# Optimization experiments

Hardware: AMD Instinct MI355X
Metric: run time of the kernel (lower is better)

## Reference

```python
import jax, jax.numpy as jnp
import numpy as np

T, B, C = 256, 32, 64          # max_time, batch, num_classes
BEAM, TOP = 16, 4              # beam_width, top_paths
BLANK = 0                      # blank_index
NEG = -1e9                     # soft -inf (keeps grads NaN-free)


def setup_inputs() -> dict:
    key = jax.random.key(0)
    k1, k2 = jax.random.split(key)
    data = jax.random.normal(k1, (T, B, C), dtype=jnp.float32)
    data_length = jax.random.randint(k2, (B,), 1, T + 1, dtype=jnp.int32)
    return {"data": data, "data_length": data_length}


def _decode_one(logp, length):
    """Graves-style CTC prefix beam search for one sample.
    logp: [T, C] log-probs, length: scalar number of valid frames.
    Beam state: padded label seqs, lengths, log p(ending in blank),
    log p(ending in non-blank), two rolling prefix hashes (for duplicate-prefix
    merging), and an 'active' flag."""
    classes = jnp.arange(C)
    seqs0 = jnp.full((BEAM, T), -1, jnp.int32)
    lens0 = jnp.zeros((BEAM,), jnp.int32)
    p_b0 = jnp.full((BEAM,), NEG, jnp.float32).at[0].set(0.0)  # empty prefix
    p_nb0 = jnp.full((BEAM,), NEG, jnp.float32)
    h1_0 = jnp.zeros((BEAM,), jnp.uint32)
    h2_0 = jnp.zeros((BEAM,), jnp.uint32)
    act0 = jnp.zeros((BEAM,), bool).at[0].set(True)

    def step(state, inp):
        seqs, lens, p_b, p_nb, h1, h2, act = state
        lp, t = inp                                   # lp: [C]
        tot = jnp.logaddexp(p_b, p_nb)                # [BEAM]
        last = seqs[jnp.arange(BEAM), jnp.maximum(lens - 1, 0)]
        last = jnp.where(lens > 0, last, -1)
        # ---- 'stay' candidates: same prefix (blank, or repeat of last char) ----
        stay_pb = tot + lp[BLANK]
        stay_pnb = jnp.where(lens > 0, p_nb + lp[jnp.maximum(last, 0)], NEG)
        # ---- 'extend' candidates: prefix + c, c != blank ----
        # repeat char only extends via a blank-ending path (p_b)
        base = jnp.where(classes[None, :] == last[:, None], p_b[:, None], tot[:, None])
        ext = base + lp[None, :]                      # [BEAM, C]
        ext = jnp.where((classes[None, :] == BLANK) | (~act[:, None]), NEG, ext)
        cc = (classes[None, :] + 1).astype(jnp.uint32)
        ch1 = h1[:, None] * jnp.uint32(1000003) + cc  # [BEAM, C]
        ch2 = h2[:, None] * jnp.uint32(69069) + cc
        # merge: extend(i,c) equal to an existing active beam j folds into j's p_nb
        match = ((ch1[:, :, None] == h1[None, None, :])
                 & (ch2[:, :, None] == h2[None, None, :])
                 & act[None, None, :])                # [BEAM, C, BEAM]
        merged = jax.nn.logsumexp(jnp.where(match, ext[:, :, None], NEG), axis=(0, 1))
        stay_pnb = jnp.logaddexp(stay_pnb, merged)
        ext = jnp.where(match.any(-1), NEG, ext)
        # ---- prune: top BEAM among BEAM stays + BEAM*C extends ----
        stay_tot = jnp.logaddexp(stay_pb, stay_pnb)
        scores = jnp.concatenate([stay_tot, ext.reshape(-1)])
        vals, idx = jax.lax.top_k(scores, BEAM)
        is_stay = idx < BEAM
        parent = jnp.where(is_stay, idx, (idx - BEAM) // C)
        c_new = jnp.where(is_stay, 0, (idx - BEAM) % C)
        plen = lens[parent]
        n_seqs = seqs[parent]
        put = (jnp.arange(T)[None, :] == plen[:, None]) & (~is_stay)[:, None]
        n_seqs = jnp.where(put, c_new[:, None].astype(jnp.int32), n_seqs)
        n_lens = plen + (~is_stay).astype(jnp.int32)
        n_pb = jnp.where(is_stay, stay_pb[parent], NEG)
        n_pnb = jnp.where(is_stay, stay_pnb[parent], vals)
        n_h1 = jnp.where(is_stay, h1[parent], ch1[parent, c_new])
        n_h2 = jnp.where(is_stay, h2[parent], ch2[parent, c_new])
        n_act = vals > NEG / 2
        live = t < length                             # freeze state past data_length
        new_state = tuple(jnp.where(live, n, o) for n, o in zip(
            (n_seqs, n_lens, n_pb, n_pnb, n_h1, n_h2, n_act),
            (seqs, lens, p_b, p_nb, h1, h2, act)))
        return new_state, None

    state, _ = jax.lax.scan(step, (seqs0, lens0, p_b0, p_nb0, h1_0, h2_0, act0),
                            (logp, jnp.arange(T)))
    seqs, lens, p_b, p_nb, _, _, _ = state
    tot = jnp.logaddexp(p_b, p_nb)
    top_tot, order = jax.lax.top_k(tot, TOP)
    # (neg log prob, label length, decoded labels padded with -1)
    return -top_tot, lens[order], seqs[order]


def reference(data, data_length):
    logp = jax.nn.log_softmax(data, axis=-1)          # from_logits=True
    logp = jnp.transpose(logp, (1, 0, 2))             # [B, T, C]
    probs, lengths, labels = jax.vmap(_decode_one)(logp, data_length)
    return probs, lengths, labels
```

## Files before the change

kernel.cpp:

```cpp
#include <hip/hip_runtime.h>


#define T_MAX 256
#define BATCH 32
#define NC 64
#define BEAM 16
#define TOPK 4
#define NEG (-1.0e9f)
#define BIGNEG (-2.0e9f)
#define FLTMAX 3.402823466e+38f

typedef unsigned long long u64;
typedef unsigned int u32;

__device__ __forceinline__ float log_add_exp(float a, float b) {
    float m = fmaxf(a, b);
    float d = fabsf(a - b);
    return m + log1pf(expf(-d));
}

__device__ __forceinline__ u32 rdl_u32(u32 v, int sl) {
    return (u32)__builtin_amdgcn_readlane((int)v, sl);
}
__device__ __forceinline__ float rdl_f(float v, int sl) {
    return __uint_as_float(rdl_u32(__float_as_uint(v), sl));
}
__device__ __forceinline__ int rdl_i(int v, int sl) {
    return __builtin_amdgcn_readlane(v, sl);
}
__device__ __forceinline__ u32 mbcnt64(u64 m) {
    return __builtin_amdgcn_mbcnt_hi((u32)(m >> 32),
           __builtin_amdgcn_mbcnt_lo((u32)m, 0u));
}

__device__ __forceinline__ u64 pack_key_fl(float v, u32 fl) {
    u32 u = __float_as_uint(v);
    u32 m = u ^ ((u32)((int)u >> 31) | 0x80000000u);
    return ((u64)m << 11) | (u64)fl;
}
__device__ __forceinline__ u64 pack_key(float v, int flat) {
    return pack_key_fl(v, (u32)(2047 - flat));
}
__device__ __forceinline__ float key_val(u64 key) {
    u32 k = (u32)(key >> 11);
    u32 u = (k & 0x80000000u) ? (k ^ 0x80000000u) : ~k;
    return __uint_as_float(u);
}
__device__ __forceinline__ int key_flat(u64 key) {
    return 2047 - (int)(key & 2047u);
}
__device__ __forceinline__ u64 max64(u64 a, u64 b) { return a > b ? a : b; }
__device__ __forceinline__ u64 min64(u64 a, u64 b) { return a < b ? a : b; }

__device__ __forceinline__ void sort16_desc_u64(u64 (&a)[BEAM]) {
    #pragma unroll
    for (int k = 2; k <= 16; k <<= 1) {
        #pragma unroll
        for (int j = k >> 1; j > 0; j >>= 1) {
            #pragma unroll
            for (int i = 0; i < 16; ++i) {
                int l = i ^ j;
                if (l > i) {
                    const bool desc = ((i & k) == 0);
                    u64 x = a[i], y = a[l];
                    bool sw = desc ? (x < y) : (x > y);
                    a[i] = sw ? y : x;
                    a[l] = sw ? x : y;
                }
            }
        }
    }
}

__device__ __forceinline__ void sort16_desc_f32(float (&a)[BEAM]) {
    #pragma unroll
    for (int k = 2; k <= 16; k <<= 1) {
        #pragma unroll
        for (int j = k >> 1; j > 0; j >>= 1) {
            #pragma unroll
            for (int i = 0; i < 16; ++i) {
                int l = i ^ j;
                if (l > i) {
                    const bool desc = ((i & k) == 0);
                    float x = a[i], y = a[l];
                    float mx = fmaxf(x, y), mn = fminf(x, y);
                    a[i] = desc ? mx : mn;
                    a[l] = desc ? mn : mx;
                }
            }
        }
    }
}

template <int M>
__device__ __forceinline__ void bf_level_f32(float (&a)[BEAM]) {
    float c[BEAM];
    #pragma unroll
    for (int i = 0; i < BEAM; ++i)
        c[i] = __shfl_xor(a[BEAM - 1 - i], M, 64);
    #pragma unroll
    for (int i = 0; i < BEAM; ++i)
        c[i] = fmaxf(a[i], c[i]);
    #pragma unroll
    for (int j = 8; j > 0; j >>= 1) {
        #pragma unroll
        for (int i = 0; i < BEAM; ++i)
            if ((i & j) == 0) {
                float x = c[i], y = c[i | j];
                c[i]     = fmaxf(x, y);
                c[i | j] = fminf(x, y);
            }
    }
    #pragma unroll
    for (int i = 0; i < BEAM; ++i) a[i] = c[i];
}

__global__ __launch_bounds__(64) void softmax_kernel(const float* __restrict__ data,
                                                     float* __restrict__ lp_out,
                                                     float* __restrict__ rm_out) {
    const int row = blockIdx.x;
    const int lane = threadIdx.x;
    float x = data[row * NC + lane];
    float mx = x;
    #pragma unroll
    for (int m = 1; m < 64; m <<= 1) mx = fmaxf(mx, __shfl_xor(mx, m, 64));
    float sum = expf(x - mx);
    #pragma unroll
    for (int m = 1; m < 64; m <<= 1) sum += __shfl_xor(sum, m, 64);
    float ls = logf(sum);
    lp_out[row * NC + lane] = (x - mx) - ls;
    if (lane == 0) rm_out[row] = -ls;
}

template <bool PRE>
__global__ __launch_bounds__(64, 1) void ctc_beam_kernel(
        const float* __restrict__ data,
        const float* __restrict__ lp_pre,
        const float* __restrict__ rm_pre,
        const int*   __restrict__ data_len,
        float*       __restrict__ out)
{
    const int b    = blockIdx.x;
    const int lane = threadIdx.x;

    __shared__ __align__(16) u64 slotsL[128];
    __shared__ unsigned short hist[T_MAX * BEAM];
    __shared__ int ord4[TOPK];
    __shared__ float val4[TOPK];

    int len = data_len[b];
    if (len < 0) len = 0;
    if (len > T_MAX) len = T_MAX;

    float pb  = (lane == 0) ? 0.0f : NEG;
    float pnb = NEG;
    float tot = log_add_exp(pb, pnb);
    u32 h1 = 0u, h2 = 0u;
    u32 ph1 = 0u, ph2 = 0u;
    int lenb = 0, lastb = -1;
    float spread = 1.0e30f;
    float v1prev = 0.0f;

    const float* src = PRE ? lp_pre : data;
    float xpref = (len > 0) ? src[b * NC + lane] : 0.f;
    float rmpref = (PRE && len > 0) ? rm_pre[b] : 0.f;

    #pragma unroll 1
    for (int t = 0; t < len; ++t) {
        float x = xpref;
        float rm = rmpref;
        int tn = (t + 1 < len) ? (t + 1) : t;
        xpref = src[(tn * BATCH + b) * NC + lane];
        if (PRE) rmpref = rm_pre[tn * BATCH + b];

        slotsL[lane] = 0ull;

        float lp;
        if (PRE) {
            lp = x;
        } else {
            float mx = x;
            #pragma unroll
            for (int m = 1; m < 64; m <<= 1) mx = fmaxf(mx, __shfl_xor(mx, m, 64));
            float sum = expf(x - mx);
            #pragma unroll
            for (int m = 1; m < 64; m <<= 1) sum += __shfl_xor(sum, m, 64);
            float ls = logf(sum);
            lp = (x - mx) - ls;
            rm = -ls;
        }
        float lp0 = rdl_f(lp, 0);

        int lastc = (lastb < 0) ? 0 : (lastb & 63);
        float lplast = __shfl(lp, lastc, 64);
        float st_pb   = tot + lp0;
        float st_pnb0 = (lenb > 0) ? (pnb + lplast) : NEG;

        u32 p2 = (h2 & 0x03FFFFFFu) | ((u32)(lastb & 63) << 26);
        u32 ph2m = ph2 & 0x03FFFFFFu;
        float lpx = (lane == 0) ? BIGNEG : lp;

        float e0s[BEAM];
        int mi = -1;
        #pragma unroll
        for (int i = 0; i < BEAM; ++i) {
            float tot_i = rdl_f(tot, i);
            float pb_i  = rdl_f(pb, i);
            u32   h1_i  = rdl_u32(h1, i);
            u32   p2_i  = rdl_u32(p2, i);
            int last_i = (int)(p2_i >> 26);
            float e0  = tot_i + lpx;
            float e0f = pb_i + lpx;
            e0s[i] = (lane == last_i) ? e0f : e0;
            if (ph1 == h1_i && ph2m == (p2_i & 0x03FFFFFFu)) mi = i;
        }

        bool jm = (lane < BEAM) && (lenb > 0) && (mi >= 0);
        u64 mm = __ballot(jm);
        float merged = NEG;
        float st_pnb;
        if (mm) {
            u32 excl = 0u;
            int mpack = ((mi & 15) << 6) | (lastb & 63);
            u64 mw = mm;
            while (mw) {
                int j = (int)__builtin_ctzll(mw);
                mw &= mw - 1;
                int pk = rdl_i(mpack, j);
                int i  = (pk >> 6) & 15;
                int c  = pk & 63;
                float tot_i = rdl_f(tot, i);
                float pb_i  = rdl_f(pb, i);
                int   l_i   = rdl_i(lastb, i);
                float lp_c  = rdl_f(lp, c);
                float mv = ((c == l_i) ? pb_i : tot_i) + lp_c;
                if (lane == j) merged = mv;
                if (lane == c) excl |= (1u << i);
            }
            #pragma unroll
            for (int s = 0; s < BEAM; ++s)
                if ((excl >> s) & 1u) e0s[s] = BIGNEG;
            st_pnb = log_add_exp(st_pnb0, merged);
        } else {
            st_pnb = st_pnb0;
        }
        float st_tot = log_add_exp(st_pb, st_pnb);

        auto do_scatter = [&](float th) -> u32 {
            u32 mycnt = 0;
            #pragma unroll
            for (int s = 0; s < BEAM; ++s) mycnt += (e0s[s] >= th) ? 1u : 0u;
            bool stw = (lane < BEAM) && (st_tot >= th);
            mycnt += stw ? 1u : 0u;
            u32 base = 0;
            #pragma unroll
            for (int k = 0; k < 5; ++k)
                base += mbcnt64(__ballot(((mycnt >> k) & 1u) != 0u)) << k;
            u32 totc = rdl_u32(base + mycnt, 63);
            u32 pos = base;
            u32 dump = (64u + (u32)lane) << 3;
            u32 fl = 2031u - (u32)lane;
            #pragma unroll
            for (int s = 0; s < BEAM; ++s) {
                bool w = (e0s[s] >= th) && (pos < 64u);
                u32 a = w ? (pos << 3) : dump;
                *(u64*)((char*)slotsL + a) = pack_key_fl(e0s[s], fl);
                pos += (e0s[s] >= th) ? 1u : 0u;
                fl -= 64u;
            }
            {
                u32 a = (stw && pos < 64u) ? (pos << 3) : dump;
                *(u64*)((char*)slotsL + a) = pack_key_fl(st_tot, 2047u - (u32)lane);
            }
            return totc;
        };

        float A = v1prev + rm;
        u32 totc = do_scatter(A - spread);
        if (totc < BEAM || totc > 32u) {
            float th2 = (totc > 32u) ? (A - 0.45f * spread)
                                     : (A - (2.5f * spread + 1.0f));
            slotsL[lane] = 0ull;
            asm volatile("" ::: "memory");
            totc = do_scatter(th2);
            if (totc < BEAM || totc > 32u) {
                float a[BEAM];
                #pragma unroll
                for (int s = 0; s < BEAM; ++s) a[s] = e0s[s];
                sort16_desc_f32(a);
                {
                    float sv = (lane < BEAM) ? st_tot : NEG;
                    #pragma unroll
                    for (int i = BEAM - 1; i >= 1; --i)
                        a[i] = fmaxf(a[i], fminf(a[i - 1], sv));
                    a[0] = fmaxf(a[0], sv);
                }
                bf_level_f32<1>(a);  bf_level_f32<2>(a);  bf_level_f32<4>(a);
                bf_level_f32<8>(a);  bf_level_f32<16>(a); bf_level_f32<32>(a);
                slotsL[lane] = 0ull;
                asm volatile("" ::: "memory");
                totc = do_scatter(a[15]);
            }
        }

        int flat; float val;
        if (totc <= 32u) {
            asm volatile("" ::: "memory");
            u64 mk = slotsL[lane];
            u32 rank = 0;
            const uint4* q4 = (const uint4*)slotsL;
            if (totc <= 16u) {
                #pragma unroll
                for (int q = 0; q < 8; ++q) {
                    uint4 w = q4[q];
                    u64 ka = ((u64)w.y << 32) | w.x;
                    u64 kb = ((u64)w.w << 32) | w.z;
                    rank += (ka > mk) ? 1u : 0u;
                    rank += (kb > mk) ? 1u : 0u;
                }
            } else {
                #pragma unroll
                for (int q = 0; q < 16; ++q) {
                    uint4 w = q4[q];
                    u64 ka = ((u64)w.y << 32) | w.x;
                    u64 kb = ((u64)w.w << 32) | w.z;
                    rank += (ka > mk) ? 1u : 0u;
                    rank += (kb > mk) ? 1u : 0u;
                }
            }
            int selhi = 0, sello = 0;
            if (lane < (int)totc) {
                selhi = __builtin_amdgcn_ds_permute((int)(rank << 2),
                                                    (int)(mk >> 32));
                sello = __builtin_amdgcn_ds_permute((int)(rank << 2),
                                                    (int)(mk & 0xFFFFFFFFu));
            }
            u64 sel = ((u64)(u32)selhi << 32) | (u32)sello;
            flat = key_flat(sel);
            val  = key_val(sel);
        } else {
            u64 ku[BEAM];
            #pragma unroll
            for (int s = 0; s < BEAM; ++s)
                ku[s] = pack_key(e0s[s], BEAM + s * NC + lane);
            sort16_desc_u64(ku);
            u64 sk = (lane < BEAM) ? pack_key(st_tot, lane) : 0ull;
            #pragma unroll
            for (int i = BEAM - 1; i >= 1; --i)
                ku[i] = max64(ku[i], min64(ku[i - 1], sk));
            ku[0] = max64(ku[0], sk);
            #pragma unroll 1
            for (int m = 1; m < 64; m <<= 1) {
                u64 c_[BEAM];
                #pragma unroll
                for (int i = 0; i < BEAM; ++i) {
                    u64 o = (u64)__shfl_xor((long long)ku[BEAM - 1 - i], m, 64);
                    c_[i] = max64(ku[i], o);
                }
                #pragma unroll
                for (int j = 8; j > 0; j >>= 1) {
                    #pragma unroll
                    for (int i = 0; i < BEAM; ++i)
                        if ((i & j) == 0) {
                            u64 xk = c_[i], yk = c_[i | j];
                            bool sw = xk < yk;
                            c_[i]     = sw ? yk : xk;
                            c_[i | j] = sw ? xk : yk;
                        }
                }
                #pragma unroll
                for (int i = 0; i < BEAM; ++i) ku[i] = c_[i];
            }
            u64 selkey = ku[0];
            #pragma unroll
            for (int i = 1; i < BEAM; ++i)
                if (lane == i) selkey = ku[i];
            flat = key_flat(selkey);
            val  = key_val(selkey);
        }

        {
            float v1n  = rdl_f(val, 0);
            float v16n = rdl_f(val, 15);
            spread = (fmaxf(A, v1n) - v16n) * 1.25f + 1.0e-3f;
            v1prev = v1n;
        }

        bool stay = flat < BEAM;
        int pidx = (stay ? flat : ((flat - BEAM) >> 6)) & 15;
        int cnew = stay ? 0 : ((flat - BEAM) & 63);

        float g_stpb  = __shfl(st_pb, pidx, 64);
        float g_stpnb = __shfl(st_pnb, pidx, 64);
        u32   g_h1    = (u32)__shfl((int)h1, pidx, 64);
        u32   g_h2    = (u32)__shfl((int)h2, pidx, 64);
        u32   g_ph1   = (u32)__shfl((int)ph1, pidx, 64);
        u32   g_ph2   = (u32)__shfl((int)ph2, pidx, 64);
        int   g_ll    = __shfl((lenb << 8) | (lastb & 255), pidx, 64);
        int   g_len   = g_ll >> 8;
        int   g_last  = (int)(signed char)(g_ll & 255);

        pb   = stay ? g_stpb : NEG;
        pnb  = stay ? g_stpnb : val;
        tot  = val;
        ph1  = stay ? g_ph1 : g_h1;
        ph2  = stay ? g_ph2 : g_h2;
        h1   = stay ? g_h1 : (g_h1 * 1000003u + (u32)(cnew + 1));
        h2   = stay ? g_h2 : (g_h2 * 69069u   + (u32)(cnew + 1));
        lenb = g_len + (stay ? 0 : 1);
        lastb = stay ? g_last : cnew;
        if (lane < BEAM)
            hist[t * BEAM + lane] =
                (unsigned short)((pidx << 8) | (stay ? 0x80 : 0) | cnew);
    }
    __syncthreads();

    float ft = (lane < BEAM) ? log_add_exp(pb, pnb) : -FLTMAX;
    int fidx = (lane < BEAM) ? lane : 0x7FFFFFFF;
    for (int k = 0; k < TOPK; ++k) {
        float bv = ft; int bi = fidx;
        #pragma unroll
        for (int m = 1; m < 64; m <<= 1) {
            float ov = __shfl_xor(bv, m, 64);
            int   oi = __shfl_xor(bi, m, 64);
            if (ov > bv || (ov == bv && oi < bi)) { bv = ov; bi = oi; }
        }
        if (lane == 0) { ord4[k] = bi; val4[k] = bv; }
        if (lane == bi) ft = -FLTMAX;
    }
    __syncthreads();

    int bsel = ord4[lane & 3] & 15;
    int lensel = __shfl(lenb, bsel, 64);

    for (int e2 = lane; e2 < TOPK * T_MAX; e2 += 64)
        out[BATCH * TOPK * 2 + b * (TOPK * T_MAX) + e2] = -1.0f;
    __syncthreads();
    if (lane < TOPK) {
        const int k = lane;
        out[b * TOPK + k] = -val4[k];
        out[BATCH * TOPK + b * TOPK + k] = (float)lensel;
        int pos = lensel - 1;
        int cur = ord4[k];
        float* lab = out + BATCH * TOPK * 2 + b * (TOPK * T_MAX) + k * T_MAX;
        for (int tt = len - 1; tt >= 0; --tt) {
            unsigned short h = hist[tt * BEAM + cur];
            if (!(h & 0x80)) { lab[pos] = (float)(h & 0x7F); --pos; }
            cur = h >> 8;
        }
    }
}

extern "C" void kernel_launch(void* const* d_in, const int* in_sizes, int n_in,
                              void* d_out, int out_size, void* d_ws, size_t ws_size,
                              hipStream_t stream) {
    const float* data = (const float*)d_in[0];
    const int* data_len = (const int*)d_in[1];
    float* out = (float*)d_out;
    const size_t lp_bytes = (size_t)T_MAX * BATCH * NC * sizeof(float);
    const size_t rm_bytes = (size_t)T_MAX * BATCH * sizeof(float);
    if (ws_size >= lp_bytes + rm_bytes) {
        float* lp_ws = (float*)d_ws;
        float* rm_ws = lp_ws + (size_t)T_MAX * BATCH * NC;
        softmax_kernel<<<dim3(T_MAX * BATCH), dim3(64), 0, stream>>>(data, lp_ws, rm_ws);
        ctc_beam_kernel<true><<<dim3(BATCH), dim3(64), 0, stream>>>(data, lp_ws, rm_ws, data_len, out);
    } else {
        ctc_beam_kernel<false><<<dim3(BATCH), dim3(64), 0, stream>>>(data, nullptr, nullptr, data_len, out);
    }
}
```

Measured before the change: 590.5 us.

## Pack beam state into fewer registers, bitmask scatter, batch softmax rows, coalesce output

Beam state now lives in a packed p2 word (26-bit hash plus last char) and a prefix mask. This drops the separate h2, ph2, lenb and lastb registers and cuts shuffles in the per-step gather. The per-lane candidate count and scatter positions come from a bitmask with popcount instead of a serial running counter. The softmax kernel processes 4 rows per 256-thread block, and label backtracking goes to shared scratch before one coalesced write of the output. Beam length is now recovered from the backtrack count, and 'has last char' is tested as lastc != 0, which relies on blank never being a last character.

```diff
diff --git a/kernel.cpp b/kernel.cpp
--- a/kernel.cpp
+++ b/kernel.cpp
@@ -9,6 +9,7 @@
 #define NEG (-1.0e9f)
 #define BIGNEG (-2.0e9f)
 #define FLTMAX 3.402823466e+38f
+#define M26 0x03FFFFFFu
 
 typedef unsigned long long u64;
 typedef unsigned int u32;
@@ -115,11 +116,11 @@
     for (int i = 0; i < BEAM; ++i) a[i] = c[i];
 }
 
-__global__ __launch_bounds__(64) void softmax_kernel(const float* __restrict__ data,
-                                                     float* __restrict__ lp_out,
-                                                     float* __restrict__ rm_out) {
-    const int row = blockIdx.x;
-    const int lane = threadIdx.x;
+__global__ __launch_bounds__(256) void softmax_kernel(const float* __restrict__ data,
+                                                      float* __restrict__ lp_out,
+                                                      float* __restrict__ rm_out) {
+    const int row = blockIdx.x * 4 + (threadIdx.x >> 6);
+    const int lane = threadIdx.x & 63;
     float x = data[row * NC + lane];
     float mx = x;
     #pragma unroll
@@ -145,8 +146,10 @@
 
     __shared__ __align__(16) u64 slotsL[128];
     __shared__ unsigned short hist[T_MAX * BEAM];
+    __shared__ unsigned char scr[TOPK * T_MAX];
     __shared__ int ord4[TOPK];
     __shared__ float val4[TOPK];
+    __shared__ int cnt4[TOPK];
 
     int len = data_len[b];
     if (len < 0) len = 0;
@@ -155,9 +158,8 @@
     float pb  = (lane == 0) ? 0.0f : NEG;
     float pnb = NEG;
     float tot = log_add_exp(pb, pnb);
-    u32 h1 = 0u, h2 = 0u;
-    u32 ph1 = 0u, ph2 = 0u;
-    int lenb = 0, lastb = -1;
+    u32 h1 = 0u, p2 = 0u;
+    u32 ph1 = 0u, ph2m = 0u;
     float spread = 1.0e30f;
     float v1prev = 0.0f;
 
@@ -191,17 +193,15 @@
         }
         float lp0 = rdl_f(lp, 0);
 
-        int lastc = (lastb < 0) ? 0 : (lastb & 63);
+        int lastc = (int)(p2 >> 26);
         float lplast = __shfl(lp, lastc, 64);
         float st_pb   = tot + lp0;
-        float st_pnb0 = (lenb > 0) ? (pnb + lplast) : NEG;
-
-        u32 p2 = (h2 & 0x03FFFFFFu) | ((u32)(lastb & 63) << 26);
-        u32 ph2m = ph2 & 0x03FFFFFFu;
+        float st_pnb0 = (lastc != 0) ? (pnb + lplast) : NEG;
+
         float lpx = (lane == 0) ? BIGNEG : lp;
 
         float e0s[BEAM];
-        int mi = -1;
+        u32 mbits = 0u;
         #pragma unroll
         for (int i = 0; i < BEAM; ++i) {
             float tot_i = rdl_f(tot, i);
@@ -209,19 +209,18 @@
             u32   h1_i  = rdl_u32(h1, i);
             u32   p2_i  = rdl_u32(p2, i);
             int last_i = (int)(p2_i >> 26);
-            float e0  = tot_i + lpx;
-            float e0f = pb_i + lpx;
-            e0s[i] = (lane == last_i) ? e0f : e0;
-            if (ph1 == h1_i && ph2m == (p2_i & 0x03FFFFFFu)) mi = i;
-        }
-
-        bool jm = (lane < BEAM) && (lenb > 0) && (mi >= 0);
+            e0s[i] = ((lane == last_i) ? pb_i : tot_i) + lpx;
+            mbits |= (ph1 == h1_i && ph2m == (p2_i & M26)) ? (1u << i) : 0u;
+        }
+
+        bool jm = (lane < BEAM) && (lastc != 0) && (mbits != 0u);
         u64 mm = __ballot(jm);
         float merged = NEG;
         float st_pnb;
         if (mm) {
             u32 excl = 0u;
-            int mpack = ((mi & 15) << 6) | (lastb & 63);
+            int mi = (int)__builtin_ctz(mbits | 0x10000u);
+            int mpack = ((mi & 15) << 6) | lastc;
             u64 mw = mm;
             while (mw) {
                 int j = (int)__builtin_ctzll(mw);
@@ -231,7 +230,7 @@
                 int c  = pk & 63;
                 float tot_i = rdl_f(tot, i);
                 float pb_i  = rdl_f(pb, i);
-                int   l_i   = rdl_i(lastb, i);
+                int   l_i   = (int)(rdl_u32(p2, i) >> 26);
                 float lp_c  = rdl_f(lp, c);
                 float mv = ((c == l_i) ? pb_i : tot_i) + lp_c;
                 if (lane == j) merged = mv;
@@ -247,29 +246,30 @@
         float st_tot = log_add_exp(st_pb, st_pnb);
 
         auto do_scatter = [&](float th) -> u32 {
-            u32 mycnt = 0;
-            #pragma unroll
-            for (int s = 0; s < BEAM; ++s) mycnt += (e0s[s] >= th) ? 1u : 0u;
+            u32 sm = 0u;
+            #pragma unroll
+            for (int s = 0; s < BEAM; ++s)
+                sm |= (e0s[s] >= th) ? (1u << s) : 0u;
             bool stw = (lane < BEAM) && (st_tot >= th);
-            mycnt += stw ? 1u : 0u;
+            u32 mycnt = (u32)__popc(sm) + (stw ? 1u : 0u);
             u32 base = 0;
             #pragma unroll
             for (int k = 0; k < 5; ++k)
                 base += mbcnt64(__ballot(((mycnt >> k) & 1u) != 0u)) << k;
             u32 totc = rdl_u32(base + mycnt, 63);
-            u32 pos = base;
             u32 dump = (64u + (u32)lane) << 3;
             u32 fl = 2031u - (u32)lane;
             #pragma unroll
             for (int s = 0; s < BEAM; ++s) {
-                bool w = (e0s[s] >= th) && (pos < 64u);
+                u32 pos = base + (u32)__popc(sm & ((1u << s) - 1u));
+                bool w = ((sm >> s) & 1u) && (pos < 64u);
                 u32 a = w ? (pos << 3) : dump;
                 *(u64*)((char*)slotsL + a) = pack_key_fl(e0s[s], fl);
-                pos += (e0s[s] >= th) ? 1u : 0u;
                 fl -= 64u;
             }
             {
-                u32 a = (stw && pos < 64u) ? (pos << 3) : dump;
+                u32 spos = base + (u32)__popc(sm);
+                u32 a = (stw && spos < 64u) ? (spos << 3) : dump;
                 *(u64*)((char*)slotsL + a) = pack_key_fl(st_tot, 2047u - (u32)lane);
             }
             return totc;
@@ -393,22 +393,19 @@
         float g_stpb  = __shfl(st_pb, pidx, 64);
         float g_stpnb = __shfl(st_pnb, pidx, 64);
         u32   g_h1    = (u32)__shfl((int)h1, pidx, 64);
-        u32   g_h2    = (u32)__shfl((int)h2, pidx, 64);
+        u32   g_p2    = (u32)__shfl((int)p2, pidx, 64);
         u32   g_ph1   = (u32)__shfl((int)ph1, pidx, 64);
-        u32   g_ph2   = (u32)__shfl((int)ph2, pidx, 64);
-        int   g_ll    = __shfl((lenb << 8) | (lastb & 255), pidx, 64);
-        int   g_len   = g_ll >> 8;
-        int   g_last  = (int)(signed char)(g_ll & 255);
+        u32   g_ph2m  = (u32)__shfl((int)ph2m, pidx, 64);
 
         pb   = stay ? g_stpb : NEG;
         pnb  = stay ? g_stpnb : val;
         tot  = val;
+        u32 h2n = (((g_p2 & M26) * 69069u + (u32)(cnew + 1)) & M26)
+                | ((u32)cnew << 26);
+        h1   = stay ? g_h1 : (g_h1 * 1000003u + (u32)(cnew + 1));
+        p2   = stay ? g_p2 : h2n;
         ph1  = stay ? g_ph1 : g_h1;
-        ph2  = stay ? g_ph2 : g_h2;
-        h1   = stay ? g_h1 : (g_h1 * 1000003u + (u32)(cnew + 1));
-        h2   = stay ? g_h2 : (g_h2 * 69069u   + (u32)(cnew + 1));
-        lenb = g_len + (stay ? 0 : 1);
-        lastb = stay ? g_last : cnew;
+        ph2m = stay ? g_ph2m : (g_p2 & M26);
         if (lane < BEAM)
             hist[t * BEAM + lane] =
                 (unsigned short)((pidx << 8) | (stay ? 0x80 : 0) | cnew);
@@ -430,24 +427,26 @@
     }
     __syncthreads();
 
-    int bsel = ord4[lane & 3] & 15;
-    int lensel = __shfl(lenb, bsel, 64);
-
-    for (int e2 = lane; e2 < TOPK * T_MAX; e2 += 64)
-        out[BATCH * TOPK * 2 + b * (TOPK * T_MAX) + e2] = -1.0f;
-    __syncthreads();
     if (lane < TOPK) {
         const int k = lane;
-        out[b * TOPK + k] = -val4[k];
-        out[BATCH * TOPK + b * TOPK + k] = (float)lensel;
-        int pos = lensel - 1;
-        int cur = ord4[k];
-        float* lab = out + BATCH * TOPK * 2 + b * (TOPK * T_MAX) + k * T_MAX;
+        int cur = ord4[k] & 15;
+        int rp = T_MAX, c = 0;
         for (int tt = len - 1; tt >= 0; --tt) {
             unsigned short h = hist[tt * BEAM + cur];
-            if (!(h & 0x80)) { lab[pos] = (float)(h & 0x7F); --pos; }
+            if (!(h & 0x80)) { scr[k * T_MAX + (--rp)] = (unsigned char)(h & 0x7F); ++c; }
             cur = h >> 8;
         }
+        cnt4[k] = c;
+        out[b * TOPK + k] = -val4[k];
+        out[BATCH * TOPK + b * TOPK + k] = (float)c;
+    }
+    __syncthreads();
+    for (int e2 = lane; e2 < TOPK * T_MAX; e2 += 64) {
+        int k = e2 >> 8;
+        int p = e2 & (T_MAX - 1);
+        int c = cnt4[k];
+        float v = (p < c) ? (float)scr[k * T_MAX + T_MAX - c + p] : -1.0f;
+        out[BATCH * TOPK * 2 + b * (TOPK * T_MAX) + k * T_MAX + p] = v;
     }
 }
 
@@ -462,7 +461,7 @@
     if (ws_size >= lp_bytes + rm_bytes) {
         float* lp_ws = (float*)d_ws;
         float* rm_ws = lp_ws + (size_t)T_MAX * BATCH * NC;
-        softmax_kernel<<<dim3(T_MAX * BATCH), dim3(64), 0, stream>>>(data, lp_ws, rm_ws);
+        softmax_kernel<<<dim3(T_MAX * BATCH / 4), dim3(256), 0, stream>>>(data, lp_ws, rm_ws);
         ctc_beam_kernel<true><<<dim3(BATCH), dim3(64), 0, stream>>>(data, lp_ws, rm_ws, data_len, out);
     } else {
         ctc_beam_kernel<false><<<dim3(BATCH), dim3(64), 0, stream>>>(data, nullptr, nullptr, data_len, out);
```

New measurement: 688.3 us. +16.6%, slower.
